# Kernel optimization log

Hardware: AMD Instinct MI355X
Metric: run time of the kernel (lower is better)

The kernel has to match this reference:

```python
import jax, jax.numpy as jnp
import numpy as np

DIM = 384
HEADS = 12
HEAD_DIM = DIM // HEADS
WIN = (2, 7, 7)
NW_TOK = WIN[0] * WIN[1] * WIN[2]  # 98
SCALE = HEAD_DIM ** -0.5


def _relative_position_index():
    d = np.arange(WIN[0]); h = np.arange(WIN[1]); w = np.arange(WIN[2])
    coords = np.stack(np.meshgrid(d, h, w, indexing='ij'))  # [3,D,H,W]
    cf = coords.reshape(3, -1)  # [3, NW_TOK]
    rel = cf[:, :, None] - cf[:, None, :]  # [3, N, N]
    rel = rel.transpose(1, 2, 0).astype(np.int64)
    rel[:, :, 0] += WIN[0] - 1
    rel[:, :, 1] += WIN[1] - 1
    rel[:, :, 2] += WIN[2] - 1
    rel[:, :, 0] *= (2 * WIN[1] - 1) * (2 * WIN[2] - 1)
    rel[:, :, 1] *= 2 * WIN[2] - 1
    return rel.sum(-1)  # [NW_TOK, NW_TOK]


def setup_inputs() -> dict:
    key = jax.random.key(0)
    ks = jax.random.split(key, 6)
    B_, N = 1024, NW_TOK + 1
    nW = 64
    table_len = (2 * WIN[0] - 1) * (2 * WIN[1] - 1) * (2 * WIN[2] - 1)  # 507
    x = jax.random.normal(ks[0], (B_, N, DIM), dtype=jnp.float32)
    mask = jax.random.normal(ks[1], (nW, NW_TOK, NW_TOK), dtype=jnp.float32)
    W_qkv = jax.random.normal(ks[2], (DIM, 3 * DIM), dtype=jnp.float32) * 0.02
    rpb_table = jax.random.normal(ks[3], (table_len, HEADS), dtype=jnp.float32) * 0.02
    W_proj = jax.random.normal(ks[4], (DIM, DIM), dtype=jnp.float32) * 0.02
    b_proj = jnp.zeros((DIM,), dtype=jnp.float32)
    rpi = jnp.asarray(_relative_position_index(), dtype=jnp.int32)
    return {"x": x, "mask": mask, "W_qkv": W_qkv, "rpb_table": rpb_table,
            "W_proj": W_proj, "b_proj": b_proj, "rpi": rpi}


def reference(x, mask, W_qkv, rpb_table, W_proj, b_proj, rpi):
    B_, N, C = x.shape
    qkv = (x @ W_qkv).reshape(B_, N, 3, HEADS, HEAD_DIM)
    q, k, v = qkv[:, :, 0], qkv[:, :, 1], qkv[:, :, 2]  # [B_, N, H, hd]
    attn = jnp.einsum('bnhd,bmhd->bhnm', q * SCALE, k)  # [B_, H, N, N]
    # gathered relative position bias over non-class tokens, zero-padded for class token
    bias = rpb_table[rpi.reshape(-1)].reshape(NW_TOK, NW_TOK, HEADS).transpose(2, 0, 1)
    bias_full = jnp.pad(bias, ((0, 0), (1, 0), (1, 0)))  # [H, N, N]
    attn = attn + bias_full[None]
    nW = mask.shape[0]
    mask_full = jnp.pad(mask, ((0, 0), (1, 0), (1, 0)))  # [nW, N, N]
    attn = attn.reshape(B_ // nW, nW, HEADS, N, N) + mask_full[None, :, None]
    attn = attn.reshape(B_, HEADS, N, N)
    attn = jax.nn.softmax(attn, axis=-1)
    out = jnp.einsum('bhnm,bmhd->bnhd', attn, v).reshape(B_, N, C)
    out = out @ W_proj + b_proj
    return out[:, 1:], out[:, :1]
```

## Files before the change

kernel.cpp:

```cpp
#include <hip/hip_runtime.h>
#include <hip/hip_bf16.h>
#include <cstddef>
#include <cstdint>


using bf16 = __hip_bfloat16;
typedef short v8s __attribute__((ext_vector_type(8)));
typedef short v4s __attribute__((ext_vector_type(4)));
typedef float v4f __attribute__((ext_vector_type(4)));

static constexpr int    NTOK   = 99;
static constexpr int    CDIM   = 384;
static constexpr int    NHEAD  = 12;
static constexpr int    NROWS  = 101376;
static constexpr size_t PLANE  = (size_t)NROWS * 32;
static constexpr float  SCALEF = 0.17677669529663687f;

__device__ __forceinline__ v4f mfma16x16x32(v8s a, v8s b, v4f c) {
  return __builtin_amdgcn_mfma_f32_16x16x32_bf16(a, b, c, 0, 0, 0);
}
__device__ __forceinline__ short f2bf(float f) {
  bf16 h = __float2bfloat16(f);
  return *reinterpret_cast<short*>(&h);
}
__device__ __forceinline__ float bf2f(short s) {
  bf16 h = *reinterpret_cast<bf16*>(&s);
  return __bfloat162float(h);
}

static constexpr size_t WT_QKV_OFF = 0;
static constexpr size_t WT_P_OFF   = 884736;
static constexpr size_t BIAS_OFF   = 884736 + 294912;
static constexpr size_t COMMON_END = 1650096;
static constexpr size_t O_WS_OFF   = COMMON_END;
static constexpr size_t WS_MID     = O_WS_OFF + (size_t)NROWS * 384 * 2;
static constexpr size_t BMF_OFF    = COMMON_END;
static constexpr size_t BMF_BYTES  = (size_t)64 * NHEAD * 7 * 7 * 64 * 4 * 2;
static constexpr size_t QKV_OFF    = BMF_OFF + BMF_BYTES;
static constexpr size_t WS_FULL    = QKV_OFF + (size_t)NROWS * 1152 * 2;

static constexpr int PREP_BASE = 1152 * 384 + 384 * 384 + NHEAD * 99 * 99;
static constexpr int PREP_BMF  = 64 * NHEAD * 7 * 7 * 64 * 4;

__global__ void prep_kernel(const float* __restrict__ Wqkv, const float* __restrict__ Wproj,
                            const float* __restrict__ rpb,  const int* __restrict__ rpi,
                            const float* __restrict__ mask,
                            bf16* __restrict__ WtQKV, bf16* __restrict__ WtP,
                            float* __restrict__ BIAS, bf16* __restrict__ BMF, int do_bmf)
{
  int idx = blockIdx.x * 256 + threadIdx.x;
  if (idx < 1152 * 384) {
    int c = idx / 384, k = idx - c * 384;
    WtQKV[idx] = __float2bfloat16(Wqkv[k * 1152 + c]);
  } else if (idx < 1152 * 384 + 384 * 384) {
    int j = idx - 1152 * 384;
    int c = j / 384, k = j - c * 384;
    WtP[j] = __float2bfloat16(Wproj[k * 384 + c]);
  } else if (idx < PREP_BASE) {
    int j = idx - (1152 * 384 + 384 * 384);
    int h = j / (99 * 99), r = j % (99 * 99);
    int nn = r / 99, mm = r % 99;
    float v = 0.f;
    if (nn > 0 && mm > 0) v = rpb[rpi[(nn - 1) * 98 + (mm - 1)] * NHEAD + h];
    BIAS[j] = v;
  } else if (do_bmf && idx < PREP_BASE + PREP_BMF) {
    int j2 = idx - PREP_BASE;
    int j    = j2 & 3;
    int lane = (j2 >> 2) & 63;
    int blk  = j2 >> 8;
    int t    = blk % 7;
    int w    = (blk / 7) % 7;
    int h    = (blk / 49) % NHEAD;
    int wi   = blk / (49 * NHEAD);
    int row = 16 * w + (lane >> 4) * 4 + j;
    int col = 16 * t + (lane & 15);
    float v = 0.f;
    if (row >= 1 && row <= 98 && col >= 1 && col <= 98)
      v = rpb[rpi[(row - 1) * 98 + (col - 1)] * NHEAD + h]
        + mask[((size_t)wi * 98 + (row - 1)) * 98 + (col - 1)];
    BMF[j2] = __float2bfloat16(v);
  }
}

static constexpr int GQ_LD    = 72;
static constexpr int GQ_OFFB  = 0;
static constexpr int GQ_OFFA  = 192 * GQ_LD * 2;
static constexpr int GQ_LDS   = GQ_OFFA + 128 * GQ_LD * 2;
static constexpr int CSTG_LD  = 104;

__global__ __launch_bounds__(512)
void k_qkv(const float* __restrict__ x, const bf16* __restrict__ WtQKV,
           bf16* __restrict__ qkv2)
{
  __shared__ __align__(16) char smem[GQ_LDS];
  bf16* B_lds = (bf16*)(smem + GQ_OFFB);
  bf16* A_lds = (bf16*)(smem + GQ_OFFA);
  bf16* C_stg = (bf16*)(smem);

  const int tid  = threadIdx.x;
  const int wave = tid >> 6;
  const int wm   = wave >> 2;
  const int wn   = wave & 3;
  const int lane = tid & 63;
  const int g    = lane >> 4;
  const int li   = lane & 15;
  const int tile = (blockIdx.x & 7) * 594 + (blockIdx.x >> 3);
  const int R0   = (tile / 6) * 128;
  const int CN   = (tile % 6) * 192;

  const int brr = tid >> 3, bk8 = tid & 7;
  const int arr = tid >> 3, ak8 = tid & 7;

  v4f acc[4][3];
  #pragma unroll
  for (int mi = 0; mi < 4; ++mi)
    #pragma unroll
    for (int ni = 0; ni < 3; ++ni) acc[mi][ni] = (v4f){0.f, 0.f, 0.f, 0.f};

  v8s breg[3];
  v4f areg[2][2];

  auto load_regs = [&](int kc) {
    const int k0 = kc * 64;
    #pragma unroll
    for (int p = 0; p < 3; ++p)
      breg[p] = *(const v8s*)(WtQKV + (size_t)(CN + brr + p * 64) * 384 + k0 + bk8 * 8);
    #pragma unroll
    for (int p = 0; p < 2; ++p) {
      const float* src = x + (size_t)(R0 + arr + p * 64) * 384 + k0 + ak8 * 8;
      areg[p][0] = *(const v4f*)(src);
      areg[p][1] = *(const v4f*)(src + 4);
    }
  };
  auto write_lds = [&]() {
    #pragma unroll
    for (int p = 0; p < 3; ++p)
      *(v8s*)(B_lds + (brr + p * 64) * GQ_LD + bk8 * 8) = breg[p];
    #pragma unroll
    for (int p = 0; p < 2; ++p) {
      v8s f;
      #pragma unroll
      for (int j = 0; j < 4; ++j) { f[j] = f2bf(areg[p][0][j]); f[j + 4] = f2bf(areg[p][1][j]); }
      *(v8s*)(A_lds + (arr + p * 64) * GQ_LD + ak8 * 8) = f;
    }
  };

  load_regs(0);
  write_lds();
  __syncthreads();

  for (int kc = 0; kc < 6; ++kc) {
    if (kc < 5) load_regs(kc + 1);
    #pragma unroll
    for (int ks = 0; ks < 2; ++ks) {
      v8s af[4], bfr[3];
      #pragma unroll
      for (int mi = 0; mi < 4; ++mi)
        af[mi] = *(const v8s*)(A_lds + (wm * 64 + mi * 16 + li) * GQ_LD + ks * 32 + g * 8);
      #pragma unroll
      for (int ni = 0; ni < 3; ++ni)
        bfr[ni] = *(const v8s*)(B_lds + (wn * 48 + ni * 16 + li) * GQ_LD + ks * 32 + g * 8);
      #pragma unroll
      for (int mi = 0; mi < 4; ++mi)
        #pragma unroll
        for (int ni = 0; ni < 3; ++ni)
          acc[mi][ni] = mfma16x16x32(af[mi], bfr[ni], acc[mi][ni]);
    }
    __syncthreads();
    if (kc < 5) {
      write_lds();
      __syncthreads();
    }
  }

  const float scale = (CN < 384) ? SCALEF : 1.f;
  const int r_ep = tid >> 2, d8 = tid & 3;
  #pragma unroll
  for (int half = 0; half < 2; ++half) {
    __syncthreads();
    if ((wn >> 1) == half) {
      #pragma unroll
      for (int mi = 0; mi < 4; ++mi)
        #pragma unroll
        for (int ni = 0; ni < 3; ++ni)
          #pragma unroll
          for (int j = 0; j < 4; ++j)
            C_stg[(wm * 64 + mi * 16 + g * 4 + j) * CSTG_LD + (wn & 1) * 48 + ni * 16 + li] =
                __float2bfloat16(acc[mi][ni][j] * scale);
    }
    __syncthreads();
    #pragma unroll
    for (int cidx = 0; cidx < 3; ++cidx) {
      int c_global = CN + half * 96 + cidx * 32;
      int seg = c_global / 384, hh = (c_global % 384) >> 5;
      bf16* plane = qkv2 + (size_t)(hh * 3 + seg) * PLANE;
      v8s val = *(const v8s*)(C_stg + r_ep * CSTG_LD + cidx * 32 + d8 * 8);
      *(v8s*)(plane + (size_t)(R0 + r_ep) * 32 + d8 * 8) = val;
    }
  }
}

static constexpr int A_VT_LD = 136;
static constexpr int A_P_LD  = 136;
static constexpr int A_OFF_V = 0;
static constexpr int A_OFF_P = A_OFF_V + 32 * A_VT_LD * 2;
static constexpr int A_LDS   = A_OFF_P + 112 * A_P_LD * 2;

__global__ __launch_bounds__(448)
void k_attn(const bf16* __restrict__ BMF, bf16* __restrict__ qkv2)
{
  __shared__ __align__(16) char smem[A_LDS];
  bf16* vT_lds = (bf16*)(smem + A_OFF_V);
  bf16* P_lds  = (bf16*)(smem + A_OFF_P);

  const int b    = blockIdx.x;
  const int h0   = blockIdx.y * 3;
  const int tid  = threadIdx.x;
  const int wave = tid >> 6;
  const int lane = tid & 63;
  const int g    = lane >> 4;
  const int li   = lane & 15;
  const int wi   = b & 63;

  for (int z = tid; z < 32 * 29; z += 448)
    vT_lds[(z / 29) * A_VT_LD + 99 + (z % 29)] = __float2bfloat16(0.f);
  for (int z = tid; z < 112 * 29; z += 448)
    P_lds[(z / 29) * A_P_LD + 99 + (z % 29)] = __float2bfloat16(0.f);

  const int r = tid >> 2, l4 = tid & 3;
  const size_t voff = ((size_t)b * NTOK + ((r > 98) ? 98 : r)) * 32 + l4 * 8;

  const int qrow = (16 * wave + li > 98) ? 98 : 16 * wave + li;
  const size_t qoff = ((size_t)b * NTOK + qrow) * 32 + g * 8;
  size_t koff[7];
  #pragma unroll
  for (int t = 0; t < 7; ++t) {
    int krow = 16 * t + li; if (krow > 98) krow = 98;
    koff[t] = ((size_t)b * NTOK + krow) * 32 + g * 8;
  }

  {
    v8s pv = *(const v8s*)(qkv2 + (size_t)(h0 * 3 + 2) * PLANE + voff);
    if (r < NTOK) {
      #pragma unroll
      for (int e = 0; e < 8; ++e)
        *(short*)(vT_lds + (l4 * 8 + e) * A_VT_LD + r) = pv[e];
    }
  }
  __syncthreads();

  for (int hi = 0; hi < 3; ++hi) {
    const int h = h0 + hi;
    v8s nv;
    if (hi < 2) nv = *(const v8s*)(qkv2 + (size_t)(h * 3 + 5) * PLANE + voff);

    const bf16* kp = qkv2 + (size_t)(h * 3 + 1) * PLANE;
    v8s kf[7];
    #pragma unroll
    for (int t = 0; t < 7; ++t) kf[t] = *(const v8s*)(kp + koff[t]);
    v8s qf = *(const v8s*)(qkv2 + (size_t)(h * 3 + 0) * PLANE + qoff);

    const bf16* bmb = BMF + ((size_t)((wi * NHEAD + h) * 7 + wave) * 7) * 256;
    v4s bmr[7];
    #pragma unroll
    for (int t = 0; t < 7; ++t)
      bmr[t] = *(const v4s*)(bmb + t * 256 + lane * 4);

    v4f sacc[7];
    #pragma unroll
    for (int t = 0; t < 7; ++t) {
      v4f z = (v4f){0.f, 0.f, 0.f, 0.f};
      sacc[t] = mfma16x16x32(qf, kf[t], z);
    }
    #pragma unroll
    for (int t = 0; t < 7; ++t) {
      int col = 16 * t + li;
      #pragma unroll
      for (int j = 0; j < 4; ++j) {
        float s = sacc[t][j];
        if (col >= NTOK) s = -1e30f;
        else             s += bf2f(bmr[t][j]);
        sacc[t][j] = s;
      }
    }
    float linv[4];
    #pragma unroll
    for (int j = 0; j < 4; ++j) {
      float m = -1e30f;
      #pragma unroll
      for (int t = 0; t < 7; ++t) m = fmaxf(m, sacc[t][j]);
      m = fmaxf(m, __shfl_xor(m, 1));
      m = fmaxf(m, __shfl_xor(m, 2));
      m = fmaxf(m, __shfl_xor(m, 4));
      m = fmaxf(m, __shfl_xor(m, 8));
      float l = 0.f;
      #pragma unroll
      for (int t = 0; t < 7; ++t) {
        float p = __expf(sacc[t][j] - m);
        sacc[t][j] = p;
        l += p;
      }
      l += __shfl_xor(l, 1);
      l += __shfl_xor(l, 2);
      l += __shfl_xor(l, 4);
      l += __shfl_xor(l, 8);
      linv[j] = 1.f / l;
      int row = 16 * wave + g * 4 + j;
      #pragma unroll
      for (int t = 0; t < 7; ++t) {
        int col = 16 * t + li;
        if (col < NTOK) P_lds[row * A_P_LD + col] = __float2bfloat16(sacc[t][j]);
      }
    }
    v4f oacc[2];
    oacc[0] = (v4f){0.f, 0.f, 0.f, 0.f};
    oacc[1] = (v4f){0.f, 0.f, 0.f, 0.f};
    #pragma unroll
    for (int ks = 0; ks < 4; ++ks) {
      v8s ap = *(const v8s*)(P_lds + (16 * wave + li) * A_P_LD + ks * 32 + g * 8);
      #pragma unroll
      for (int t = 0; t < 2; ++t) {
        v8s bv = *(const v8s*)(vT_lds + (16 * t + li) * A_VT_LD + ks * 32 + g * 8);
        oacc[t] = mfma16x16x32(ap, bv, oacc[t]);
      }
    }
    bf16* oplane = qkv2 + (size_t)(h * 3) * PLANE;
    #pragma unroll
    for (int t = 0; t < 2; ++t) {
      #pragma unroll
      for (int j = 0; j < 4; ++j) {
        int row = 16 * wave + g * 4 + j;
        if (row < NTOK)
          oplane[((size_t)b * NTOK + row) * 32 + 16 * t + li] =
              __float2bfloat16(oacc[t][j] * linv[j]);
      }
    }
    __syncthreads();
    if (hi < 2) {
      if (r < NTOK) {
        #pragma unroll
        for (int e = 0; e < 8; ++e)
          *(short*)(vT_lds + (l4 * 8 + e) * A_VT_LD + r) = nv[e];
      }
      __syncthreads();
    }
  }
}

static constexpr int K2_LD   = 72;
static constexpr int K2_OFFW = 0;
static constexpr int K2_OFFO = 192 * K2_LD * 2;
static constexpr int K2_LDS  = K2_OFFO + 128 * K2_LD * 2;

__global__ __launch_bounds__(512)
void k2_proj(const bf16* __restrict__ O_src, const int hm,
             const bf16* __restrict__ WtP, const float* __restrict__ bproj,
             float* __restrict__ out)
{
  __shared__ __align__(16) char smem[K2_LDS];
  bf16* W_lds = (bf16*)(smem + K2_OFFW);
  bf16* O_lds = (bf16*)(smem + K2_OFFO);

  const int tid  = threadIdx.x;
  const int wave = tid >> 6;
  const int wm   = wave >> 2;
  const int wn   = wave & 3;
  const int lane = tid & 63;
  const int g    = lane >> 4;
  const int li   = lane & 15;
  const int tile = (blockIdx.x & 7) * 198 + (blockIdx.x >> 3);
  const int R0   = (tile >> 1) * 128;
  const int CN   = (tile & 1) * 192;

  v4f acc[4][3];
  #pragma unroll
  for (int mi = 0; mi < 4; ++mi)
    #pragma unroll
    for (int ni = 0; ni < 3; ++ni) acc[mi][ni] = (v4f){0.f, 0.f, 0.f, 0.f};

  for (int kc = 0; kc < 6; ++kc) {
    const int k0 = kc * 64;
    #pragma unroll
    for (int p = 0; p < 3; ++p) {
      int it = tid + p * 512, rr = it >> 3, k8 = it & 7;
      *(v8s*)(W_lds + rr * K2_LD + k8 * 8) =
          *(const v8s*)(WtP + (size_t)(CN + rr) * CDIM + k0 + k8 * 8);
    }
    #pragma unroll
    for (int p = 0; p < 2; ++p) {
      int it = tid + p * 512, rr = it >> 3, k8 = it & 7;
      const bf16* src;
      if (hm) {
        int c = k0 + k8 * 8, hh = c >> 5, d = c & 31;
        src = O_src + (size_t)(hh * 3) * PLANE + (size_t)(R0 + rr) * 32 + d;
      } else {
        src = O_src + (size_t)(R0 + rr) * 384 + k0 + k8 * 8;
      }
      *(v8s*)(O_lds + rr * K2_LD + k8 * 8) = *(const v8s*)src;
    }
    __syncthreads();
    #pragma unroll
    for (int ks = 0; ks < 2; ++ks) {
      v8s af[4], bfr[3];
      #pragma unroll
      for (int mi = 0; mi < 4; ++mi)
        af[mi] = *(const v8s*)(O_lds + (wm * 64 + mi * 16 + li) * K2_LD + ks * 32 + g * 8);
      #pragma unroll
      for (int ni = 0; ni < 3; ++ni)
        bfr[ni] = *(const v8s*)(W_lds + (wn * 48 + ni * 16 + li) * K2_LD + ks * 32 + g * 8);
      #pragma unroll
      for (int mi = 0; mi < 4; ++mi)
        #pragma unroll
        for (int ni = 0; ni < 3; ++ni)
          acc[mi][ni] = mfma16x16x32(af[mi], bfr[ni], acc[mi][ni]);
    }
    __syncthreads();
  }

  const size_t OUT2 = (size_t)1024 * 98 * CDIM;
  #pragma unroll
  for (int mi = 0; mi < 4; ++mi)
    #pragma unroll
    for (int ni = 0; ni < 3; ++ni) {
      int col = CN + wn * 48 + ni * 16 + li;
      float bb = bproj[col];
      #pragma unroll
      for (int j = 0; j < 4; ++j) {
        int rr = R0 + wm * 64 + mi * 16 + g * 4 + j;
        int b = rr / 99, n = rr - b * 99;
        float v = acc[mi][ni][j] + bb;
        if (n == 0) out[OUT2 + (size_t)b * CDIM + col] = v;
        else        out[((size_t)b * 98 + (n - 1)) * CDIM + col] = v;
      }
    }
}

static constexpr int QK_LD = 40;
static constexpr int VT_LD = 136;
static constexpr int P_LD  = 136;
static constexpr int WS_LD = 104;
static constexpr int K1_OFF_Q = 0;
static constexpr int K1_OFF_K = K1_OFF_Q + 112 * QK_LD * 2;
static constexpr int K1_OFF_V = K1_OFF_K + 112 * QK_LD * 2;
static constexpr int K1_OFF_P = K1_OFF_V + 32  * VT_LD * 2;
static constexpr int K1_OFF_W = K1_OFF_P + 112 * P_LD  * 2;
static constexpr int K1_LDS   = K1_OFF_W + 96 * WS_LD * 2;

__global__ __launch_bounds__(512)
void k1_attn(const float* __restrict__ x, const float* __restrict__ mask,
             const float* __restrict__ BIAS, const bf16* __restrict__ WtQKV,
             bf16* __restrict__ O_ws)
{
  __shared__ __align__(16) char smem[K1_LDS];
  bf16* q_lds  = (bf16*)(smem + K1_OFF_Q);
  bf16* k_lds  = (bf16*)(smem + K1_OFF_K);
  bf16* vT_lds = (bf16*)(smem + K1_OFF_V);
  bf16* P_lds  = (bf16*)(smem + K1_OFF_P);
  bf16* w_lds  = (bf16*)(smem + K1_OFF_W);

  const int b    = blockIdx.x;
  const int tid  = threadIdx.x;
  const int wave = tid >> 6;
  const int lane = tid & 63;
  const int g    = lane >> 4;
  const int li   = lane & 15;
  const int wi   = b & 63;

  v8s afr[12];
  if (wave < 7) {
    int arow = 16 * wave + li; if (arow > 98) arow = 98;
    const float* xb = x + ((size_t)b * NTOK + arow) * CDIM + g * 8;
    #pragma unroll
    for (int s = 0; s < 12; ++s) {
      v4f x0 = *(const v4f*)(xb + s * 32);
      v4f x1 = *(const v4f*)(xb + s * 32 + 4);
      v8s f;
      #pragma unroll
      for (int j = 0; j < 4; ++j) { f[j] = f2bf(x0[j]); f[j + 4] = f2bf(x1[j]); }
      afr[s] = f;
    }
  }

  for (int h = 0; h < NHEAD; ++h) {
    v4f qacc[6];
    #pragma unroll
    for (int t = 0; t < 6; ++t) qacc[t] = (v4f){0.f, 0.f, 0.f, 0.f};
    #pragma unroll
    for (int c4 = 0; c4 < 4; ++c4) {
      for (int idx = tid; idx < 96 * 12; idx += 512) {
        int rr = idx / 12, ch = idx - rr * 12;
        int cg = (rr < 32) ? (h * 32 + rr)
               : (rr < 64) ? (CDIM + h * 32 + rr - 32)
                           : (2 * CDIM + h * 32 + rr - 64);
        *(v8s*)(w_lds + rr * WS_LD + ch * 8) =
            *(const v8s*)(WtQKV + (size_t)cg * CDIM + c4 * 96 + ch * 8);
      }
      __syncthreads();
      if (wave < 7) {
        #pragma unroll
        for (int ss = 0; ss < 3; ++ss) {
          const int s = c4 * 3 + ss;
          #pragma unroll
          for (int t = 0; t < 6; ++t) {
            v8s bw = *(const v8s*)(w_lds + (16 * t + li) * WS_LD + ss * 32 + g * 8);
            qacc[t] = mfma16x16x32(afr[s], bw, qacc[t]);
          }
        }
      }
      __syncthreads();
    }
    if (wave < 7) {
      #pragma unroll
      for (int t = 0; t < 6; ++t) {
        #pragma unroll
        for (int j = 0; j < 4; ++j) {
          int row = 16 * wave + g * 4 + j;
          int col = 16 * (t & 1) + li;
          float v = qacc[t][j];
          if (t < 2)      q_lds[row * QK_LD + col] = __float2bfloat16(v * SCALEF);
          else if (t < 4) k_lds[row * QK_LD + col] = __float2bfloat16(v);
          else            vT_lds[col * VT_LD + row] = __float2bfloat16(v);
        }
      }
    }
    vT_lds[(tid >> 4) * VT_LD + 112 + (tid & 15)] = __float2bfloat16(0.f);
    __syncthreads();

    if (wave < 7) {
      v8s aq = *(const v8s*)(q_lds + (16 * wave + li) * QK_LD + g * 8);
      v4f sacc[7];
      #pragma unroll
      for (int t = 0; t < 7; ++t) {
        v8s bk = *(const v8s*)(k_lds + (16 * t + li) * QK_LD + g * 8);
        v4f z = (v4f){0.f, 0.f, 0.f, 0.f};
        sacc[t] = mfma16x16x32(aq, bk, z);
      }
      #pragma unroll
      for (int t = 0; t < 7; ++t) {
        int col = 16 * t + li;
        #pragma unroll
        for (int j = 0; j < 4; ++j) {
          int row = 16 * wave + g * 4 + j;
          float s = sacc[t][j];
          if (col >= NTOK) s = -1e30f;
          else if (row < NTOK) {
            s += BIAS[(h * NTOK + row) * NTOK + col];
            if (row > 0 && col > 0)
              s += mask[((size_t)wi * 98 + (row - 1)) * 98 + (col - 1)];
          }
          sacc[t][j] = s;
        }
      }
      float linv[4];
      #pragma unroll
      for (int j = 0; j < 4; ++j) {
        float m = -1e30f;
        #pragma unroll
        for (int t = 0; t < 7; ++t) m = fmaxf(m, sacc[t][j]);
        m = fmaxf(m, __shfl_xor(m, 1));
        m = fmaxf(m, __shfl_xor(m, 2));
        m = fmaxf(m, __shfl_xor(m, 4));
        m = fmaxf(m, __shfl_xor(m, 8));
        float l = 0.f;
        #pragma unroll
        for (int t = 0; t < 7; ++t) {
          float p = __expf(sacc[t][j] - m);
          sacc[t][j] = p;
          l += p;
        }
        l += __shfl_xor(l, 1);
        l += __shfl_xor(l, 2);
        l += __shfl_xor(l, 4);
        l += __shfl_xor(l, 8);
        linv[j] = 1.f / l;
        int row = 16 * wave + g * 4 + j;
        #pragma unroll
        for (int t = 0; t < 7; ++t)
          P_lds[row * P_LD + 16 * t + li] = __float2bfloat16(sacc[t][j]);
        P_lds[row * P_LD + 112 + li] = __float2bfloat16(0.f);
      }
      v4f oacc[2];
      oacc[0] = (v4f){0.f, 0.f, 0.f, 0.f};
      oacc[1] = (v4f){0.f, 0.f, 0.f, 0.f};
      #pragma unroll
      for (int ks = 0; ks < 4; ++ks) {
        v8s ap = *(const v8s*)(P_lds + (16 * wave + li) * P_LD + ks * 32 + g * 8);
        #pragma unroll
        for (int t = 0; t < 2; ++t) {
          v8s bv = *(const v8s*)(vT_lds + (16 * t + li) * VT_LD + ks * 32 + g * 8);
          oacc[t] = mfma16x16x32(ap, bv, oacc[t]);
        }
      }
      #pragma unroll
      for (int t = 0; t < 2; ++t) {
        #pragma unroll
        for (int j = 0; j < 4; ++j) {
          int row = 16 * wave + g * 4 + j;
          if (row < NTOK)
            O_ws[((size_t)b * 99 + row) * CDIM + h * 32 + 16 * t + li] =
                __float2bfloat16(oacc[t][j] * linv[j]);
        }
      }
    }
    __syncthreads();
  }
}

static constexpr int M_O_LD = 392;
static constexpr int M_OFF_O = 0;
static constexpr int M_OFF_Q = M_OFF_O + 99  * M_O_LD * 2;
static constexpr int M_OFF_K = M_OFF_Q + 112 * QK_LD * 2;
static constexpr int M_OFF_V = M_OFF_K + 112 * QK_LD * 2;
static constexpr int M_OFF_P = M_OFF_V + 32  * VT_LD * 2;
static constexpr int M_OFF_W = M_OFF_P + 112 * P_LD  * 2;
static constexpr int M_LDS   = M_OFF_W + 96 * WS_LD * 2;

__global__ __launch_bounds__(512)
void fused_mono(const float* __restrict__ x, const float* __restrict__ mask,
                const float* __restrict__ bproj, const float* __restrict__ BIAS,
                const bf16* __restrict__ WtQKV, const bf16* __restrict__ WtP,
                float* __restrict__ out)
{
  __shared__ __align__(16) char smem[M_LDS];
  bf16* O_lds  = (bf16*)(smem + M_OFF_O);
  bf16* q_lds  = (bf16*)(smem + M_OFF_Q);
  bf16* k_lds  = (bf16*)(smem + M_OFF_K);
  bf16* vT_lds = (bf16*)(smem + M_OFF_V);
  bf16* P_lds  = (bf16*)(smem + M_OFF_P);
  bf16* w_lds  = (bf16*)(smem + M_OFF_W);

  const int b    = blockIdx.x;
  const int tid  = threadIdx.x;
  const int wave = tid >> 6;
  const int lane = tid & 63;
  const int g    = lane >> 4;
  const int li   = lane & 15;
  const int wi   = b & 63;

  v8s afr[12];
  if (wave < 7) {
    int arow = 16 * wave + li; if (arow > 98) arow = 98;
    const float* xb = x + ((size_t)b * NTOK + arow) * CDIM + g * 8;
    #pragma unroll
    for (int s = 0; s < 12; ++s) {
      v4f x0 = *(const v4f*)(xb + s * 32);
      v4f x1 = *(const v4f*)(xb + s * 32 + 4);
      v8s f;
      #pragma unroll
      for (int j = 0; j < 4; ++j) { f[j] = f2bf(x0[j]); f[j + 4] = f2bf(x1[j]); }
      afr[s] = f;
    }
  }

  for (int h = 0; h < NHEAD; ++h) {
    v4f qacc[6];
    #pragma unroll
    for (int t = 0; t < 6; ++t) qacc[t] = (v4f){0.f, 0.f, 0.f, 0.f};
    #pragma unroll
    for (int c4 = 0; c4 < 4; ++c4) {
      for (int idx = tid; idx < 96 * 12; idx += 512) {
        int rr = idx / 12, ch = idx - rr * 12;
        int cg = (rr < 32) ? (h * 32 + rr)
               : (rr < 64) ? (CDIM + h * 32 + rr - 32)
                           : (2 * CDIM + h * 32 + rr - 64);
        *(v8s*)(w_lds + rr * WS_LD + ch * 8) =
            *(const v8s*)(WtQKV + (size_t)cg * CDIM + c4 * 96 + ch * 8);
      }
      __syncthreads();
      if (wave < 7) {
        #pragma unroll
        for (int ss = 0; ss < 3; ++ss) {
          const int s = c4 * 3 + ss;
          #pragma unroll
          for (int t = 0; t < 6; ++t) {
            v8s bw = *(const v8s*)(w_lds + (16 * t + li) * WS_LD + ss * 32 + g * 8);
            qacc[t] = mfma16x16x32(afr[s], bw, qacc[t]);
          }
        }
      }
      __syncthreads();
    }
    if (wave < 7) {
      #pragma unroll
      for (int t = 0; t < 6; ++t) {
        #pragma unroll
        for (int j = 0; j < 4; ++j) {
          int row = 16 * wave + g * 4 + j;
          int col = 16 * (t & 1) + li;
          float v = qacc[t][j];
          if (t < 2)      q_lds[row * QK_LD + col] = __float2bfloat16(v * SCALEF);
          else if (t < 4) k_lds[row * QK_LD + col] = __float2bfloat16(v);
          else            vT_lds[col * VT_LD + row] = __float2bfloat16(v);
        }
      }
    }
    vT_lds[(tid >> 4) * VT_LD + 112 + (tid & 15)] = __float2bfloat16(0.f);
    __syncthreads();

    if (wave < 7) {
      v8s aq = *(const v8s*)(q_lds + (16 * wave + li) * QK_LD + g * 8);
      v4f sacc[7];
      #pragma unroll
      for (int t = 0; t < 7; ++t) {
        v8s bk = *(const v8s*)(k_lds + (16 * t + li) * QK_LD + g * 8);
        v4f z = (v4f){0.f, 0.f, 0.f, 0.f};
        sacc[t] = mfma16x16x32(aq, bk, z);
      }
      #pragma unroll
      for (int t = 0; t < 7; ++t) {
        int col = 16 * t + li;
        #pragma unroll
        for (int j = 0; j < 4; ++j) {
          int row = 16 * wave + g * 4 + j;
          float s = sacc[t][j];
          if (col >= NTOK) s = -1e30f;
          else if (row < NTOK) {
            s += BIAS[(h * NTOK + row) * NTOK + col];
            if (row > 0 && col > 0)
              s += mask[((size_t)wi * 98 + (row - 1)) * 98 + (col - 1)];
          }
          sacc[t][j] = s;
        }
      }
      float linv[4];
      #pragma unroll
      for (int j = 0; j < 4; ++j) {
        float m = -1e30f;
        #pragma unroll
        for (int t = 0; t < 7; ++t) m = fmaxf(m, sacc[t][j]);
        m = fmaxf(m, __shfl_xor(m, 1));
        m = fmaxf(m, __shfl_xor(m, 2));
        m = fmaxf(m, __shfl_xor(m, 4));
        m = fmaxf(m, __shfl_xor(m, 8));
        float l = 0.f;
        #pragma unroll
        for (int t = 0; t < 7; ++t) {
          float p = __expf(sacc[t][j] - m);
          sacc[t][j] = p;
          l += p;
        }
        l += __shfl_xor(l, 1);
        l += __shfl_xor(l, 2);
        l += __shfl_xor(l, 4);
        l += __shfl_xor(l, 8);
        linv[j] = 1.f / l;
        int row = 16 * wave + g * 4 + j;
        #pragma unroll
        for (int t = 0; t < 7; ++t)
          P_lds[row * P_LD + 16 * t + li] = __float2bfloat16(sacc[t][j]);
        P_lds[row * P_LD + 112 + li] = __float2bfloat16(0.f);
      }
      v4f oacc[2];
      oacc[0] = (v4f){0.f, 0.f, 0.f, 0.f};
      oacc[1] = (v4f){0.f, 0.f, 0.f, 0.f};
      #pragma unroll
      for (int ks = 0; ks < 4; ++ks) {
        v8s ap = *(const v8s*)(P_lds + (16 * wave + li) * P_LD + ks * 32 + g * 8);
        #pragma unroll
        for (int t = 0; t < 2; ++t) {
          v8s bv = *(const v8s*)(vT_lds + (16 * t + li) * VT_LD + ks * 32 + g * 8);
          oacc[t] = mfma16x16x32(ap, bv, oacc[t]);
        }
      }
      #pragma unroll
      for (int t = 0; t < 2; ++t) {
        #pragma unroll
        for (int j = 0; j < 4; ++j) {
          int row = 16 * wave + g * 4 + j;
          if (row < NTOK)
            O_lds[row * M_O_LD + h * 32 + 16 * t + li] =
                __float2bfloat16(oacc[t][j] * linv[j]);
        }
      }
    }
    __syncthreads();
  }

  const size_t OUT2 = (size_t)1024 * 98 * CDIM;
  const int orow_clamped = (16 * wave + li > 98) ? 98 : 16 * wave + li;
  for (int cc = 0; cc < 4; ++cc) {
    v4f pacc[6];
    #pragma unroll
    for (int t = 0; t < 6; ++t) pacc[t] = (v4f){0.f, 0.f, 0.f, 0.f};
    for (int c4 = 0; c4 < 4; ++c4) {
      for (int idx = tid; idx < 96 * 12; idx += 512) {
        int rr = idx / 12, ch = idx - rr * 12;
        *(v8s*)(w_lds + rr * WS_LD + ch * 8) =
            *(const v8s*)(WtP + ((size_t)(cc * 96 + rr)) * CDIM + c4 * 96 + ch * 8);
      }
      __syncthreads();
      if (wave < 7) {
        #pragma unroll
        for (int ss = 0; ss < 3; ++ss) {
          const int s = c4 * 3 + ss;
          v8s ao = *(const v8s*)(O_lds + orow_clamped * M_O_LD + s * 32 + g * 8);
          #pragma unroll
          for (int t = 0; t < 6; ++t) {
            v8s bw = *(const v8s*)(w_lds + (16 * t + li) * WS_LD + ss * 32 + g * 8);
            pacc[t] = mfma16x16x32(ao, bw, pacc[t]);
          }
        }
      }
      __syncthreads();
    }
    if (wave < 7) {
      #pragma unroll
      for (int t = 0; t < 6; ++t) {
        #pragma unroll
        for (int j = 0; j < 4; ++j) {
          int row = 16 * wave + g * 4 + j;
          if (row < NTOK) {
            int col = cc * 96 + 16 * t + li;
            float v = pacc[t][j] + bproj[col];
            if (row == 0) out[OUT2 + (size_t)b * CDIM + col] = v;
            else          out[((size_t)b * 98 + (row - 1)) * CDIM + col] = v;
          }
        }
      }
    }
  }
}

extern "C" void kernel_launch(void* const* d_in, const int* in_sizes, int n_in,
                              void* d_out, int out_size, void* d_ws, size_t ws_size,
                              hipStream_t stream) {
  const float* x     = (const float*)d_in[0];
  const float* mask  = (const float*)d_in[1];
  const float* Wqkv  = (const float*)d_in[2];
  const float* rpb   = (const float*)d_in[3];
  const float* Wproj = (const float*)d_in[4];
  const float* bproj = (const float*)d_in[5];
  const int*   rpi   = (const int*)d_in[6];

  bf16*  WtQKV = (bf16*)((char*)d_ws + WT_QKV_OFF);
  bf16*  WtP   = (bf16*)((char*)d_ws + WT_P_OFF);
  float* BIAS  = (float*)((char*)d_ws + BIAS_OFF);
  bf16*  BMF   = (bf16*)((char*)d_ws + BMF_OFF);

  const bool full = (ws_size >= WS_FULL);
  const int prep_items = full ? (PREP_BASE + PREP_BMF) : PREP_BASE;
  prep_kernel<<<(prep_items + 255) / 256, 256, 0, stream>>>(
      Wqkv, Wproj, rpb, rpi, mask, WtQKV, WtP, BIAS, BMF, full ? 1 : 0);

  if (full) {
    bf16* qkv2 = (bf16*)((char*)d_ws + QKV_OFF);
    k_qkv<<<792 * 6, 512, 0, stream>>>(x, WtQKV, qkv2);
    k_attn<<<dim3(1024, 4), 448, 0, stream>>>(BMF, qkv2);
    k2_proj<<<792 * 2, 512, 0, stream>>>(qkv2, 1, WtP, bproj, (float*)d_out);
  } else if (ws_size >= WS_MID) {
    bf16* O_ws = (bf16*)((char*)d_ws + O_WS_OFF);
    k1_attn<<<1024, 512, 0, stream>>>(x, mask, BIAS, WtQKV, O_ws);
    k2_proj<<<792 * 2, 512, 0, stream>>>(O_ws, 0, WtP, bproj, (float*)d_out);
  } else {
    fused_mono<<<1024, 512, 0, stream>>>(x, mask, bproj, BIAS, WtQKV, WtP,
                                         (float*)d_out);
  }
}
```

Before: 440.5 us.

## Load QKV weights via global_load_lds, restructure bias prep, defer attention stores

The QKV GEMM now streams weight tiles straight into LDS with global_load_lds, using an XOR swizzle instead of padded rows, and restructures the k-loop so A conversion and the B load share one barrier. The prep kernel computes the bias+mask table with one thread per (window,row,col) that loops over heads, which cuts repeated rpi and mask gathers. The attention kernel buffers all three heads' outputs in registers and writes them after the loop. The aim is lower register staging and global overhead, at the cost of more live registers and reliance on the builtin being available.

```diff
diff --git a/kernel.cpp b/kernel.cpp
--- a/kernel.cpp
+++ b/kernel.cpp
@@ -26,6 +26,25 @@
 __device__ __forceinline__ float bf2f(short s) {
   bf16 h = *reinterpret_cast<bf16*>(&s);
   return __bfloat162float(h);
+}
+
+#if defined(__has_builtin)
+#if __has_builtin(__builtin_amdgcn_global_load_lds)
+#define HAS_GLL 1
+#endif
+#endif
+#ifndef HAS_GLL
+#define HAS_GLL 0
+#endif
+
+__device__ __forceinline__ void gload_lds16(const bf16* gsrc, bf16* ldst, int lane) {
+#if HAS_GLL
+  __builtin_amdgcn_global_load_lds(
+      (const __attribute__((address_space(1))) void*)gsrc,
+      (__attribute__((address_space(3))) void*)ldst, 16, 0, 0);
+#else
+  *(v8s*)(ldst + lane * 8) = *(const v8s*)gsrc;
+#endif
 }
 
 static constexpr size_t WT_QKV_OFF = 0;
@@ -40,7 +59,7 @@
 static constexpr size_t WS_FULL    = QKV_OFF + (size_t)NROWS * 1152 * 2;
 
 static constexpr int PREP_BASE = 1152 * 384 + 384 * 384 + NHEAD * 99 * 99;
-static constexpr int PREP_BMF  = 64 * NHEAD * 7 * 7 * 64 * 4;
+static constexpr int PREP_BMF2 = 64 * 112 * 112;
 
 __global__ void prep_kernel(const float* __restrict__ Wqkv, const float* __restrict__ Wproj,
                             const float* __restrict__ rpb,  const int* __restrict__ rpi,
@@ -63,38 +82,41 @@
     float v = 0.f;
     if (nn > 0 && mm > 0) v = rpb[rpi[(nn - 1) * 98 + (mm - 1)] * NHEAD + h];
     BIAS[j] = v;
-  } else if (do_bmf && idx < PREP_BASE + PREP_BMF) {
-    int j2 = idx - PREP_BASE;
-    int j    = j2 & 3;
-    int lane = (j2 >> 2) & 63;
-    int blk  = j2 >> 8;
-    int t    = blk % 7;
-    int w    = (blk / 7) % 7;
-    int h    = (blk / 49) % NHEAD;
-    int wi   = blk / (49 * NHEAD);
-    int row = 16 * w + (lane >> 4) * 4 + j;
-    int col = 16 * t + (lane & 15);
-    float v = 0.f;
-    if (row >= 1 && row <= 98 && col >= 1 && col <= 98)
-      v = rpb[rpi[(row - 1) * 98 + (col - 1)] * NHEAD + h]
-        + mask[((size_t)wi * 98 + (row - 1)) * 98 + (col - 1)];
-    BMF[j2] = __float2bfloat16(v);
-  }
-}
-
-static constexpr int GQ_LD    = 72;
-static constexpr int GQ_OFFB  = 0;
-static constexpr int GQ_OFFA  = 192 * GQ_LD * 2;
-static constexpr int GQ_LDS   = GQ_OFFA + 128 * GQ_LD * 2;
+  } else if (do_bmf && idx < PREP_BASE + PREP_BMF2) {
+    int j2  = idx - PREP_BASE;
+    int col = j2 % 112;
+    int r2  = j2 / 112;
+    int row = r2 % 112;
+    int wi  = r2 / 112;
+    int w = row >> 4, g = (row >> 2) & 3, jj = row & 3;
+    int t = col >> 4, li = col & 15, lane = g * 16 + li;
+    bool in = (row >= 1 && row <= 98 && col >= 1 && col <= 98);
+    int tix = 0; float mval = 0.f;
+    if (in) {
+      tix  = rpi[(row - 1) * 98 + (col - 1)];
+      mval = mask[((size_t)wi * 98 + (row - 1)) * 98 + (col - 1)];
+    }
+    size_t base = (((size_t)wi * NHEAD * 7 + w) * 7 + t) * 256 + lane * 4 + jj;
+    #pragma unroll
+    for (int h = 0; h < NHEAD; ++h) {
+      float v = in ? (rpb[tix * NHEAD + h] + mval) : 0.f;
+      BMF[base + (size_t)h * 12544] = __float2bfloat16(v);
+    }
+  }
+}
+
+static constexpr int GQB_OFF  = 0;
+static constexpr int GQA_OFF  = 24576;
+static constexpr int GQ_LDS2  = GQA_OFF + 128 * 72 * 2;
 static constexpr int CSTG_LD  = 104;
 
 __global__ __launch_bounds__(512)
 void k_qkv(const float* __restrict__ x, const bf16* __restrict__ WtQKV,
            bf16* __restrict__ qkv2)
 {
-  __shared__ __align__(16) char smem[GQ_LDS];
-  bf16* B_lds = (bf16*)(smem + GQ_OFFB);
-  bf16* A_lds = (bf16*)(smem + GQ_OFFA);
+  __shared__ __align__(16) char smem[GQ_LDS2];
+  bf16* B_lds = (bf16*)(smem + GQB_OFF);
+  bf16* A_lds = (bf16*)(smem + GQA_OFF);
   bf16* C_stg = (bf16*)(smem);
 
   const int tid  = threadIdx.x;
@@ -108,7 +130,6 @@
   const int R0   = (tile / 6) * 128;
   const int CN   = (tile % 6) * 192;
 
-  const int brr = tid >> 3, bk8 = tid & 7;
   const int arr = tid >> 3, ak8 = tid & 7;
 
   v4f acc[4][3];
@@ -117,14 +138,9 @@
     #pragma unroll
     for (int ni = 0; ni < 3; ++ni) acc[mi][ni] = (v4f){0.f, 0.f, 0.f, 0.f};
 
-  v8s breg[3];
   v4f areg[2][2];
-
-  auto load_regs = [&](int kc) {
+  auto load_areg = [&](int kc) {
     const int k0 = kc * 64;
-    #pragma unroll
-    for (int p = 0; p < 3; ++p)
-      breg[p] = *(const v8s*)(WtQKV + (size_t)(CN + brr + p * 64) * 384 + k0 + bk8 * 8);
     #pragma unroll
     for (int p = 0; p < 2; ++p) {
       const float* src = x + (size_t)(R0 + arr + p * 64) * 384 + k0 + ak8 * 8;
@@ -132,34 +148,43 @@
       areg[p][1] = *(const v4f*)(src + 4);
     }
   };
-  auto write_lds = [&]() {
-    #pragma unroll
-    for (int p = 0; p < 3; ++p)
-      *(v8s*)(B_lds + (brr + p * 64) * GQ_LD + bk8 * 8) = breg[p];
+  auto write_alds = [&]() {
     #pragma unroll
     for (int p = 0; p < 2; ++p) {
       v8s f;
       #pragma unroll
       for (int j = 0; j < 4; ++j) { f[j] = f2bf(areg[p][0][j]); f[j + 4] = f2bf(areg[p][1][j]); }
-      *(v8s*)(A_lds + (arr + p * 64) * GQ_LD + ak8 * 8) = f;
+      *(v8s*)(A_lds + (arr + p * 64) * 72 + ak8 * 8) = f;
     }
   };
 
-  load_regs(0);
-  write_lds();
-  __syncthreads();
+  load_areg(0);
 
   for (int kc = 0; kc < 6; ++kc) {
-    if (kc < 5) load_regs(kc + 1);
+    const int k0 = kc * 64;
+    write_alds();
+    #pragma unroll
+    for (int p = 0; p < 3; ++p) {
+      int q   = wave * 3 + p;
+      int row = q * 8 + (lane >> 3);
+      int c   = (lane & 7) ^ (row & 7);
+      const bf16* gsrc = WtQKV + (size_t)(CN + row) * 384 + k0 + c * 8;
+      gload_lds16(gsrc, B_lds + q * 512, lane);
+    }
+    if (kc < 5) load_areg(kc + 1);
+    __syncthreads();
     #pragma unroll
     for (int ks = 0; ks < 2; ++ks) {
       v8s af[4], bfr[3];
       #pragma unroll
       for (int mi = 0; mi < 4; ++mi)
-        af[mi] = *(const v8s*)(A_lds + (wm * 64 + mi * 16 + li) * GQ_LD + ks * 32 + g * 8);
-      #pragma unroll
-      for (int ni = 0; ni < 3; ++ni)
-        bfr[ni] = *(const v8s*)(B_lds + (wn * 48 + ni * 16 + li) * GQ_LD + ks * 32 + g * 8);
+        af[mi] = *(const v8s*)(A_lds + (wm * 64 + mi * 16 + li) * 72 + ks * 32 + g * 8);
+      #pragma unroll
+      for (int ni = 0; ni < 3; ++ni) {
+        int brow = wn * 48 + ni * 16 + li;
+        int sc   = (g + 4 * ks) ^ (brow & 7);
+        bfr[ni]  = *(const v8s*)(B_lds + brow * 64 + sc * 8);
+      }
       #pragma unroll
       for (int mi = 0; mi < 4; ++mi)
         #pragma unroll
@@ -167,10 +192,6 @@
           acc[mi][ni] = mfma16x16x32(af[mi], bfr[ni], acc[mi][ni]);
     }
     __syncthreads();
-    if (kc < 5) {
-      write_lds();
-      __syncthreads();
-    }
   }
 
   const float scale = (CN < 384) ? SCALEF : 1.f;
@@ -249,6 +270,9 @@
   }
   __syncthreads();
 
+  v4f oaccs[3][2];
+
+  #pragma unroll
   for (int hi = 0; hi < 3; ++hi) {
     const int h = h0 + hi;
     v8s nv;
@@ -324,26 +348,35 @@
         oacc[t] = mfma16x16x32(ap, bv, oacc[t]);
       }
     }
-    bf16* oplane = qkv2 + (size_t)(h * 3) * PLANE;
-    #pragma unroll
-    for (int t = 0; t < 2; ++t) {
+    #pragma unroll
+    for (int t = 0; t < 2; ++t)
+      #pragma unroll
+      for (int j = 0; j < 4; ++j)
+        oaccs[hi][t][j] = oacc[t][j] * linv[j];
+
+    __syncthreads();
+    if (hi < 2) {
+      if (r < NTOK) {
+        #pragma unroll
+        for (int e = 0; e < 8; ++e)
+          *(short*)(vT_lds + (l4 * 8 + e) * A_VT_LD + r) = nv[e];
+      }
+      __syncthreads();
+    }
+  }
+
+  #pragma unroll
+  for (int hi = 0; hi < 3; ++hi) {
+    bf16* oplane = qkv2 + (size_t)((h0 + hi) * 3) * PLANE;
+    #pragma unroll
+    for (int t = 0; t < 2; ++t)
       #pragma unroll
       for (int j = 0; j < 4; ++j) {
         int row = 16 * wave + g * 4 + j;
         if (row < NTOK)
           oplane[((size_t)b * NTOK + row) * 32 + 16 * t + li] =
-              __float2bfloat16(oacc[t][j] * linv[j]);
-      }
-    }
-    __syncthreads();
-    if (hi < 2) {
-      if (r < NTOK) {
-        #pragma unroll
-        for (int e = 0; e < 8; ++e)
-          *(short*)(vT_lds + (l4 * 8 + e) * A_VT_LD + r) = nv[e];
-      }
-      __syncthreads();
-    }
+              __float2bfloat16(oaccs[hi][t][j]);
+      }
   }
 }
 
@@ -838,7 +871,7 @@
   bf16*  BMF   = (bf16*)((char*)d_ws + BMF_OFF);
 
   const bool full = (ws_size >= WS_FULL);
-  const int prep_items = full ? (PREP_BASE + PREP_BMF) : PREP_BASE;
+  const int prep_items = full ? (PREP_BASE + PREP_BMF2) : PREP_BASE;
   prep_kernel<<<(prep_items + 255) / 256, 256, 0, stream>>>(
       Wqkv, Wproj, rpb, rpi, mask, WtQKV, WtP, BIAS, BMF, full ? 1 : 0);
 
```

After: 434.1 us. About the same (-1.5%).
